# Kernel tuning notes

Hardware: AMD Instinct MI355X
Metric: run time of the kernel (lower is better)

The kernel has to match this reference:

```python
import jax, jax.numpy as jnp
import numpy as np

IH, IW = 48, 48           # img_size
C = 256                   # inp == oup
NH, HD = 8, 32            # num_heads, head_dims; inner_dim = 256
HID = 4 * C               # MLP hidden
N = IH * IW               # window size (seq len) = 2304
SCALE = (C // NH) ** -0.5 # (inp_dims // num_heads) ** -0.5
EPS = 1e-5


def _relative_position_index():
    coords = np.stack(np.meshgrid(np.arange(IH), np.arange(IW), indexing='ij'))
    cf = coords.reshape(2, -1)
    rel = (cf[:, :, None] - cf[:, None, :]).transpose(1, 2, 0)
    rel[:, :, 0] += IH - 1
    rel[:, :, 1] += IW - 1
    rel[:, :, 0] *= 2 * IW - 1
    return jnp.asarray(rel.sum(-1).astype(np.int32))  # [N, N]


def setup_inputs() -> dict:
    key = jax.random.key(0)
    ks = jax.random.split(key, 12)
    s = 0.02
    return {
        'x': jax.random.normal(ks[0], (1, IH, IW, C), jnp.float32),
        'gamma1': jnp.ones((C,), jnp.float32),
        'beta1': jnp.zeros((C,), jnp.float32),
        'w_qkv': jax.random.normal(ks[1], (C, 3 * NH * HD), jnp.float32) * s,
        'w_proj': jax.random.normal(ks[2], (NH * HD, C), jnp.float32) * s,
        'b_proj': jnp.zeros((C,), jnp.float32),
        'bias_table': jax.random.normal(ks[3], ((2 * IH - 1) * (2 * IW - 1), NH), jnp.float32) * s,
        'gamma2': jnp.ones((C,), jnp.float32),
        'beta2': jnp.zeros((C,), jnp.float32),
        'w_fc1': jax.random.normal(ks[4], (C, HID), jnp.float32) * s,
        'b_fc1': jnp.zeros((HID,), jnp.float32),
        'w_fc2': jax.random.normal(ks[5], (HID, C), jnp.float32) * s,
        'b_fc2': jnp.zeros((C,), jnp.float32),
        'rel_idx': _relative_position_index(),
    }


def _layernorm(x, g, b):
    mu = jnp.mean(x, axis=-1, keepdims=True)
    var = jnp.mean(jnp.square(x - mu), axis=-1, keepdims=True)
    return (x - mu) * jax.lax.rsqrt(var + EPS) * g + b


def reference(x, gamma1, beta1, w_qkv, w_proj, b_proj, bias_table,
              gamma2, beta2, w_fc1, b_fc1, w_fc2, b_fc2, rel_idx):
    shortcut = x                                   # [1, IH, IW, C]
    t = x.reshape(1, N, C)
    t = _layernorm(t, gamma1, beta1)

    # qkv: [1, N, 3*NH*HD] -> q, k, v each [1, NH, N, HD]
    qkv = (t @ w_qkv).reshape(1, N, 3, NH, HD).transpose(2, 0, 3, 1, 4)
    q, k, v = qkv[0], qkv[1], qkv[2]
    q = q * SCALE

    attn = jnp.einsum('bhnd,bhmd->bhnm', q, k)     # [1, NH, N, N]
    # relative position bias: gather table rows by index -> [NH, N, N]
    bias = bias_table[rel_idx.reshape(-1)].reshape(N, N, NH).transpose(2, 0, 1)
    attn = jax.nn.softmax(attn + bias[None], axis=-1)

    o = jnp.einsum('bhnm,bhmd->bhnd', attn, v)     # [1, NH, N, HD]
    o = o.transpose(0, 2, 1, 3).reshape(1, N, NH * HD)
    o = o @ w_proj + b_proj                        # [1, N, C]

    x = shortcut + o.reshape(1, IH, IW, C)
    shortcut = x

    t = _layernorm(x.reshape(1, N, C), gamma2, beta2)
    t = jax.nn.gelu(t @ w_fc1 + b_fc1, approximate=False) @ w_fc2 + b_fc2
    return shortcut + t.reshape(1, IH, IW, C)
```

## Files before the change

kernel.cpp:

```cpp
#include <hip/hip_runtime.h>
#include <hip/hip_bf16.h>
#include <math.h>

#define IH 48
#define IW 48
#define NN 2304
#define CC 256
#define NH 8
#define HD 32
#define HID 1024
#define NBIAS 9025
#define SCALE 0.17677669529663687f
#define LOG2E 1.4426950408889634f
#define LN_EPS 1e-5f

typedef __attribute__((ext_vector_type(8))) short bf16x8;
typedef __attribute__((ext_vector_type(4))) short bf16x4;
typedef __attribute__((ext_vector_type(4))) float f32x4;

__device__ __forceinline__ short f2b(float f) {
    __hip_bfloat16 h = __float2bfloat16(f);
    short s; __builtin_memcpy(&s, &h, 2); return s;
}
__device__ __forceinline__ float b2f(short s) {
    __hip_bfloat16 h; __builtin_memcpy(&h, &s, 2); return __bfloat162float(h);
}
__device__ __forceinline__ float fast_exp2(float x) {
#if __has_builtin(__builtin_amdgcn_exp2f)
    return __builtin_amdgcn_exp2f(x);
#else
    return exp2f(x);
#endif
}

__global__ void prep_kernel(const float* __restrict__ x, const float* __restrict__ g,
                            const float* __restrict__ b, short* __restrict__ t1,
                            const float* __restrict__ w_qkv, const float* __restrict__ w_proj,
                            const float* __restrict__ w_fc1, const float* __restrict__ w_fc2,
                            const float* __restrict__ bt,
                            short* __restrict__ o_qkv, short* __restrict__ o_proj,
                            short* __restrict__ o_fc1, short* __restrict__ o_fc2,
                            short* __restrict__ o_bias)
{
    const int bid = blockIdx.x, tid = threadIdx.x;
    if (bid < NN) {
        __shared__ float red[8];
        float v = x[bid * CC + tid];
        float s = v, s2 = v * v;
        #pragma unroll
        for (int off = 32; off > 0; off >>= 1) {
            s  += __shfl_xor(s, off);
            s2 += __shfl_xor(s2, off);
        }
        const int wid = tid >> 6;
        if ((tid & 63) == 0) { red[wid * 2] = s; red[wid * 2 + 1] = s2; }
        __syncthreads();
        float tot  = red[0] + red[2] + red[4] + red[6];
        float tot2 = red[1] + red[3] + red[5] + red[7];
        float mu   = tot * (1.0f / CC);
        float var  = tot2 * (1.0f / CC) - mu * mu;
        float rstd = rsqrtf(var + LN_EPS);
        t1[bid * CC + tid] = f2b((v - mu) * rstd * g[tid] + b[tid]);
        return;
    }
    const int stride = (gridDim.x - NN) * 256;
    for (int i = (bid - NN) * 256 + tid; i < 858632; i += stride) {
        int j = i;
        if (j < 196608)            { int n = j >> 8,  k = j & 255;  o_qkv [j] = f2b(w_qkv [k * 768  + n]); }
        else if ((j -= 196608) < 65536)  { int n = j >> 8,  k = j & 255;  o_proj[j] = f2b(w_proj[k * 256  + n]); }
        else if ((j -= 65536)  < 262144) { int n = j >> 8,  k = j & 255;  o_fc1 [j] = f2b(w_fc1 [k * 1024 + n]); }
        else if ((j -= 262144) < 262144) { int n = j >> 10, k = j & 1023; o_fc2 [j] = f2b(w_fc2 [k * 256  + n]); }
        else { j -= 262144; int h = j / NBIAS, idx = j - h * NBIAS; o_bias[j] = f2b(bt[idx * NH + h] * LOG2E); }
    }
}

__global__ void ln_kernel(const float* __restrict__ x,
                          const float* __restrict__ g,
                          const float* __restrict__ b,
                          short* __restrict__ out)
{
    __shared__ float red[8];
    const int row = blockIdx.x, tid = threadIdx.x;
    float v = x[row * CC + tid];
    float s = v, s2 = v * v;
    #pragma unroll
    for (int off = 32; off > 0; off >>= 1) {
        s  += __shfl_xor(s, off);
        s2 += __shfl_xor(s2, off);
    }
    const int wid = tid >> 6;
    if ((tid & 63) == 0) { red[wid * 2] = s; red[wid * 2 + 1] = s2; }
    __syncthreads();
    float tot  = red[0] + red[2] + red[4] + red[6];
    float tot2 = red[1] + red[3] + red[5] + red[7];
    float mu   = tot * (1.0f / CC);
    float var  = tot2 * (1.0f / CC) - mu * mu;
    float rstd = rsqrtf(var + LN_EPS);
    out[row * CC + tid] = f2b((v - mu) * rstd * g[tid] + b[tid]);
}

#define GSTRIDE 72
template<int K>
__device__ __forceinline__ void mfma_gemm_core(const short* __restrict__ A,
                                               const short* __restrict__ BT,
                                               int m0, int n0, f32x4 acc[4],
                                               short* lds)
{
    short* As = lds;
    short* Bs = lds + 64 * GSTRIDE;
    const int tid  = threadIdx.x;
    const int w    = tid >> 6, lane = tid & 63;
    const int quad = lane >> 4, l15 = lane & 15;
    const int sr = tid >> 2;
    const int sc = (tid & 3) * 16;
    #pragma unroll
    for (int c = 0; c < 4; ++c) acc[c] = (f32x4){0.f, 0.f, 0.f, 0.f};

    const short* Ap = &A [(m0 + sr) * K + sc];
    const short* Bp = &BT[(n0 + sr) * K + sc];
    bf16x8 ra0 = *(const bf16x8*)Ap,       ra1 = *(const bf16x8*)(Ap + 8);
    bf16x8 rb0 = *(const bf16x8*)Bp,       rb1 = *(const bf16x8*)(Bp + 8);

    for (int k0 = 0; k0 < K; k0 += 64) {
        __syncthreads();
        *(bf16x8*)&As[sr * GSTRIDE + sc]     = ra0;
        *(bf16x8*)&As[sr * GSTRIDE + sc + 8] = ra1;
        *(bf16x8*)&Bs[sr * GSTRIDE + sc]     = rb0;
        *(bf16x8*)&Bs[sr * GSTRIDE + sc + 8] = rb1;
        if (k0 + 64 < K) {
            ra0 = *(const bf16x8*)(Ap + k0 + 64);
            ra1 = *(const bf16x8*)(Ap + k0 + 72);
            rb0 = *(const bf16x8*)(Bp + k0 + 64);
            rb1 = *(const bf16x8*)(Bp + k0 + 72);
        }
        __syncthreads();
        #pragma unroll
        for (int s = 0; s < 2; ++s) {
            bf16x8 a = *(const bf16x8*)&As[(w * 16 + l15) * GSTRIDE + s * 32 + quad * 8];
            #pragma unroll
            for (int c = 0; c < 4; ++c) {
                bf16x8 b = *(const bf16x8*)&Bs[(c * 16 + l15) * GSTRIDE + s * 32 + quad * 8];
                acc[c] = __builtin_amdgcn_mfma_f32_16x16x32_bf16(a, b, acc[c], 0, 0, 0);
            }
        }
    }
}

__global__ void qkv_kernel(const short* __restrict__ t1, const short* __restrict__ wT,
                           short* __restrict__ qb, short* __restrict__ kb,
                           short* __restrict__ vT)
{
    __shared__ short lds[2 * 64 * GSTRIDE];
    f32x4 acc[4];
    const int m0 = blockIdx.y * 64, n0 = blockIdx.x * 64;
    mfma_gemm_core<256>(t1, wT, m0, n0, acc, lds);
    const int lane = threadIdx.x & 63, w = threadIdx.x >> 6;
    const int quad = lane >> 4, l15 = lane & 15;
    #pragma unroll
    for (int c = 0; c < 4; ++c) {
        int col = n0 + c * 16 + l15;
        int three = col >> 8, rem = col & 255;
        int h = rem >> 5, d = rem & 31;
        #pragma unroll
        for (int r = 0; r < 4; ++r) {
            int row = m0 + w * 16 + quad * 4 + r;
            float v = acc[c][r];
            if (three == 0)      qb[(h * NN + row) * HD + d] = f2b(v * (SCALE * LOG2E));
            else if (three == 1) kb[(h * NN + row) * HD + d] = f2b(v);
            else                 vT[(h * HD + d) * NN + row] = f2b(v);
        }
    }
}

__global__ __launch_bounds__(256) void attn_kernel(
        const short* __restrict__ qb, const short* __restrict__ kb,
        const short* __restrict__ vT, const short* __restrict__ biasT,
        short* __restrict__ o)
{
    __shared__ float Ored[4][16][33];
    __shared__ float lred[4][16];
    const int w = threadIdx.x >> 6, lane = threadIdx.x & 63;
    const int quad = lane >> 4, l15 = lane & 15;
    const int h = blockIdx.x / 144, q0 = (blockIdx.x % 144) * 16;
    const int t0 = w * 576;
    const short* bt = &biasT[h * NBIAS];

    bf16x8 qf = *(const bf16x8*)&qb[(h * NN + q0 + l15) * HD + quad * 8];

    const int qi = q0 / IW, qj = (q0 % IW) + l15;
    const int qbase = (qi + 47) * 95 + (qj + 47);

    f32x4 O0 = (f32x4){0.f,0.f,0.f,0.f}, O1 = (f32x4){0.f,0.f,0.f,0.f};
    float lp = 0.f;
    const f32x4 zero = (f32x4){0.f,0.f,0.f,0.f};

    for (int c = 0; c < 18; ++c) {
        const int t = t0 + c * 32;
        bf16x8 k0f = *(const bf16x8*)&kb[(h * NN + t      + l15) * HD + quad * 8];
        bf16x8 k1f = *(const bf16x8*)&kb[(h * NN + t + 16 + l15) * HD + quad * 8];
        const short* vp0 = &vT[(h * HD + l15)      * NN + t + quad * 4];
        const short* vp1 = &vT[(h * HD + 16 + l15) * NN + t + quad * 4];
        bf16x4 va0 = *(const bf16x4*)vp0, vb0 = *(const bf16x4*)(vp0 + 16);
        bf16x4 va1 = *(const bf16x4*)vp1, vb1 = *(const bf16x4*)(vp1 + 16);

        f32x4 s0 = __builtin_amdgcn_mfma_f32_16x16x32_bf16(k0f, qf, zero, 0, 0, 0);
        f32x4 s1 = __builtin_amdgcn_mfma_f32_16x16x32_bf16(k1f, qf, zero, 0, 0, 0);

        const int kA = t + quad * 4;
        const int kiA = kA / IW, kjA = kA % IW;
        const int kB = kA + 16;
        const int kiB = kB / IW, kjB = kB % IW;
        const short* pA = bt + (qbase - (kiA * 95 + kjA));
        const short* pB = bt + (qbase - (kiB * 95 + kjB));

        float p[8];
        #pragma unroll
        for (int r = 0; r < 4; ++r) {
            p[r]     = fast_exp2(s0[r] + b2f(pA[-r]));
            p[4 + r] = fast_exp2(s1[r] + b2f(pB[-r]));
        }
        #pragma unroll
        for (int r = 0; r < 8; ++r) lp += p[r];
        bf16x8 pa = (bf16x8){ f2b(p[0]), f2b(p[1]), f2b(p[2]), f2b(p[3]),
                              f2b(p[4]), f2b(p[5]), f2b(p[6]), f2b(p[7]) };
        bf16x8 v0 = (bf16x8){ va0[0], va0[1], va0[2], va0[3],
                              vb0[0], vb0[1], vb0[2], vb0[3] };
        bf16x8 v1 = (bf16x8){ va1[0], va1[1], va1[2], va1[3],
                              vb1[0], vb1[1], vb1[2], vb1[3] };
        O0 = __builtin_amdgcn_mfma_f32_16x16x32_bf16(pa, v0, O0, 0, 0, 0);
        O1 = __builtin_amdgcn_mfma_f32_16x16x32_bf16(pa, v1, O1, 0, 0, 0);
    }

    lp += __shfl_xor(lp, 16);
    lp += __shfl_xor(lp, 32);
    if (quad == 0) lred[w][l15] = lp;
    #pragma unroll
    for (int r = 0; r < 4; ++r) {
        Ored[w][quad * 4 + r][l15]      = O0[r];
        Ored[w][quad * 4 + r][16 + l15] = O1[r];
    }
    __syncthreads();
    {
        const int col = threadIdx.x & 31;
        for (int rr = threadIdx.x >> 5; rr < 16; rr += 8) {
            float s = 0.f, l = 0.f;
            #pragma unroll
            for (int pw = 0; pw < 4; ++pw) { s += Ored[pw][rr][col]; l += lred[pw][rr]; }
            o[(q0 + rr) * CC + h * HD + col] = f2b(s / l);
        }
    }
}

__global__ void proj_kernel(const short* __restrict__ o, const short* __restrict__ wT,
                            const float* __restrict__ bias, const float* __restrict__ x_in,
                            float* __restrict__ x2)
{
    __shared__ short lds[2 * 64 * GSTRIDE];
    f32x4 acc[4];
    const int m0 = blockIdx.y * 64, n0 = blockIdx.x * 64;
    mfma_gemm_core<256>(o, wT, m0, n0, acc, lds);
    const int lane = threadIdx.x & 63, w = threadIdx.x >> 6;
    const int quad = lane >> 4, l15 = lane & 15;
    #pragma unroll
    for (int c = 0; c < 4; ++c) {
        int col = n0 + c * 16 + l15;
        #pragma unroll
        for (int r = 0; r < 4; ++r) {
            int row = m0 + w * 16 + quad * 4 + r;
            x2[row * CC + col] = acc[c][r] + bias[col] + x_in[row * CC + col];
        }
    }
}

__global__ void fc1_kernel(const short* __restrict__ t2, const short* __restrict__ wT,
                           const float* __restrict__ bias, short* __restrict__ h1)
{
    __shared__ short lds[2 * 64 * GSTRIDE];
    f32x4 acc[4];
    const int m0 = blockIdx.y * 64, n0 = blockIdx.x * 64;
    mfma_gemm_core<256>(t2, wT, m0, n0, acc, lds);
    const int lane = threadIdx.x & 63, w = threadIdx.x >> 6;
    const int quad = lane >> 4, l15 = lane & 15;
    #pragma unroll
    for (int c = 0; c < 4; ++c) {
        int col = n0 + c * 16 + l15;
        #pragma unroll
        for (int r = 0; r < 4; ++r) {
            int row = m0 + w * 16 + quad * 4 + r;
            float v = acc[c][r] + bias[col];
            float ge = 0.5f * v * (1.0f + erff(v * 0.7071067811865476f));
            h1[row * HID + col] = f2b(ge);
        }
    }
}

__global__ void fc2_kernel(const short* __restrict__ h1, const short* __restrict__ wT,
                           const float* __restrict__ bias, const float* __restrict__ x2,
                           float* __restrict__ out)
{
    __shared__ short lds[2 * 64 * GSTRIDE];
    f32x4 acc[4];
    const int m0 = blockIdx.y * 64, n0 = blockIdx.x * 64;
    mfma_gemm_core<1024>(h1, wT, m0, n0, acc, lds);
    const int lane = threadIdx.x & 63, w = threadIdx.x >> 6;
    const int quad = lane >> 4, l15 = lane & 15;
    #pragma unroll
    for (int c = 0; c < 4; ++c) {
        int col = n0 + c * 16 + l15;
        #pragma unroll
        for (int r = 0; r < 4; ++r) {
            int row = m0 + w * 16 + quad * 4 + r;
            out[row * CC + col] = acc[c][r] + bias[col] + x2[row * CC + col];
        }
    }
}

extern "C" void kernel_launch(void* const* d_in, const int* in_sizes, int n_in,
                              void* d_out, int out_size, void* d_ws, size_t ws_size,
                              hipStream_t stream)
{
    const float* x          = (const float*)d_in[0];
    const float* gamma1     = (const float*)d_in[1];
    const float* beta1      = (const float*)d_in[2];
    const float* w_qkv      = (const float*)d_in[3];
    const float* w_proj     = (const float*)d_in[4];
    const float* b_proj     = (const float*)d_in[5];
    const float* bias_table = (const float*)d_in[6];
    const float* gamma2     = (const float*)d_in[7];
    const float* beta2      = (const float*)d_in[8];
    const float* w_fc1      = (const float*)d_in[9];
    const float* b_fc1      = (const float*)d_in[10];
    const float* w_fc2      = (const float*)d_in[11];
    const float* b_fc2      = (const float*)d_in[12];

    short* S = (short*)d_ws;
    const int NC = NN * CC;
    short* t1     = S;
    short* qb     = t1  + NC;
    short* kb     = qb  + NC;
    short* vT     = kb  + NC;
    short* obuf   = vT  + NC;
    short* t2     = obuf+ NC;
    short* h1     = t2  + NC;
    short* wTqkv  = h1  + NN * HID;
    short* wTproj = wTqkv  + 768 * 256;
    short* wTfc1  = wTproj + 256 * 256;
    short* wTfc2  = wTfc1  + 1024 * 256;
    short* biasT  = wTfc2  + 256 * 1024;
    float* x2     = (float*)(biasT + NH * NBIAS + 8);

    prep_kernel<<<NN + 512, 256, 0, stream>>>(x, gamma1, beta1, t1,
                                              w_qkv, w_proj, w_fc1, w_fc2, bias_table,
                                              wTqkv, wTproj, wTfc1, wTfc2, biasT);
    qkv_kernel<<<dim3(12, 36), 256, 0, stream>>>(t1, wTqkv, qb, kb, vT);
    attn_kernel<<<1152, 256, 0, stream>>>(qb, kb, vT, biasT, obuf);
    proj_kernel<<<dim3(4, 36), 256, 0, stream>>>(obuf, wTproj, b_proj, x, x2);
    ln_kernel<<<NN, 256, 0, stream>>>(x2, gamma2, beta2, t2);
    fc1_kernel<<<dim3(16, 36), 256, 0, stream>>>(t2, wTfc1, b_fc1, h1);
    fc2_kernel<<<dim3(4, 36), 256, 0, stream>>>(h1, wTfc2, b_fc2, x2,
                                                (float*)d_out);
}
```

Measured before the change: 187.9 us.

## Split attention key range across three blocks and reduce partials in separate kernel

The attention kernel now splits the key sequence three ways (split-K / flash-decoding style), launching three times as many blocks, each covering a third of the keys. Partial unnormalized outputs and row sums go to fp32 workspace, and a new normalization kernel sums the partials and divides. The relative-position bias table is also stored as fp32 instead of bf16, which removes the bf16-to-float conversion in the inner loop. In exchange there is an extra kernel launch, extra global traffic for the fp32 partials, and a larger bias table to read.

```diff
diff --git a/kernel.cpp b/kernel.cpp
--- a/kernel.cpp
+++ b/kernel.cpp
@@ -13,6 +13,7 @@
 #define SCALE 0.17677669529663687f
 #define LOG2E 1.4426950408889634f
 #define LN_EPS 1e-5f
+#define NSPLIT 3
 
 typedef __attribute__((ext_vector_type(8))) short bf16x8;
 typedef __attribute__((ext_vector_type(4))) short bf16x4;
@@ -40,7 +41,7 @@
                             const float* __restrict__ bt,
                             short* __restrict__ o_qkv, short* __restrict__ o_proj,
                             short* __restrict__ o_fc1, short* __restrict__ o_fc2,
-                            short* __restrict__ o_bias)
+                            float* __restrict__ o_bias)
 {
     const int bid = blockIdx.x, tid = threadIdx.x;
     if (bid < NN) {
@@ -70,7 +71,7 @@
         else if ((j -= 196608) < 65536)  { int n = j >> 8,  k = j & 255;  o_proj[j] = f2b(w_proj[k * 256  + n]); }
         else if ((j -= 65536)  < 262144) { int n = j >> 8,  k = j & 255;  o_fc1 [j] = f2b(w_fc1 [k * 1024 + n]); }
         else if ((j -= 262144) < 262144) { int n = j >> 10, k = j & 1023; o_fc2 [j] = f2b(w_fc2 [k * 256  + n]); }
-        else { j -= 262144; int h = j / NBIAS, idx = j - h * NBIAS; o_bias[j] = f2b(bt[idx * NH + h] * LOG2E); }
+        else { j -= 262144; int h = j / NBIAS, idx = j - h * NBIAS; o_bias[j] = bt[idx * NH + h] * LOG2E; }
     }
 }
 
@@ -174,16 +175,18 @@
 
 __global__ __launch_bounds__(256) void attn_kernel(
         const short* __restrict__ qb, const short* __restrict__ kb,
-        const short* __restrict__ vT, const short* __restrict__ biasT,
-        short* __restrict__ o)
+        const short* __restrict__ vT, const float* __restrict__ biasF,
+        float* __restrict__ Opart, float* __restrict__ lpart)
 {
     __shared__ float Ored[4][16][33];
     __shared__ float lred[4][16];
     const int w = threadIdx.x >> 6, lane = threadIdx.x & 63;
     const int quad = lane >> 4, l15 = lane & 15;
-    const int h = blockIdx.x / 144, q0 = (blockIdx.x % 144) * 16;
-    const int t0 = w * 576;
-    const short* bt = &biasT[h * NBIAS];
+    const int sp = blockIdx.x / 1152;
+    const int bb = blockIdx.x - sp * 1152;
+    const int h = bb / 144, q0 = (bb % 144) * 16;
+    const int t0 = sp * (NN / NSPLIT) + w * (NN / NSPLIT / 4);
+    const float* bt = &biasF[h * NBIAS];
 
     bf16x8 qf = *(const bf16x8*)&qb[(h * NN + q0 + l15) * HD + quad * 8];
 
@@ -194,7 +197,7 @@
     float lp = 0.f;
     const f32x4 zero = (f32x4){0.f,0.f,0.f,0.f};
 
-    for (int c = 0; c < 18; ++c) {
+    for (int c = 0; c < 6; ++c) {
         const int t = t0 + c * 32;
         bf16x8 k0f = *(const bf16x8*)&kb[(h * NN + t      + l15) * HD + quad * 8];
         bf16x8 k1f = *(const bf16x8*)&kb[(h * NN + t + 16 + l15) * HD + quad * 8];
@@ -207,17 +210,15 @@
         f32x4 s1 = __builtin_amdgcn_mfma_f32_16x16x32_bf16(k1f, qf, zero, 0, 0, 0);
 
         const int kA = t + quad * 4;
-        const int kiA = kA / IW, kjA = kA % IW;
         const int kB = kA + 16;
-        const int kiB = kB / IW, kjB = kB % IW;
-        const short* pA = bt + (qbase - (kiA * 95 + kjA));
-        const short* pB = bt + (qbase - (kiB * 95 + kjB));
+        const float* pA = bt + (qbase - ((kA / IW) * 95 + kA % IW));
+        const float* pB = bt + (qbase - ((kB / IW) * 95 + kB % IW));
 
         float p[8];
         #pragma unroll
         for (int r = 0; r < 4; ++r) {
-            p[r]     = fast_exp2(s0[r] + b2f(pA[-r]));
-            p[4 + r] = fast_exp2(s1[r] + b2f(pB[-r]));
+            p[r]     = fast_exp2(s0[r] + pA[-r]);
+            p[4 + r] = fast_exp2(s1[r] + pB[-r]);
         }
         #pragma unroll
         for (int r = 0; r < 8; ++r) lp += p[r];
@@ -246,9 +247,22 @@
             float s = 0.f, l = 0.f;
             #pragma unroll
             for (int pw = 0; pw < 4; ++pw) { s += Ored[pw][rr][col]; l += lred[pw][rr]; }
-            o[(q0 + rr) * CC + h * HD + col] = f2b(s / l);
-        }
-    }
+            Opart[sp * (NN * CC) + (q0 + rr) * CC + h * HD + col] = s;
+            if (col == 0) lpart[(sp * NH + h) * NN + q0 + rr] = l;
+        }
+    }
+}
+
+__global__ void attn_norm_kernel(const float* __restrict__ Opart,
+                                 const float* __restrict__ lpart,
+                                 short* __restrict__ obuf)
+{
+    const int n = blockIdx.x, c = threadIdx.x, h = c >> 5;
+    float v = Opart[n * CC + c] + Opart[NN * CC + n * CC + c]
+            + Opart[2 * NN * CC + n * CC + c];
+    float l = lpart[h * NN + n] + lpart[(NH + h) * NN + n]
+            + lpart[(2 * NH + h) * NN + n];
+    obuf[n * CC + c] = f2b(v / l);
 }
 
 __global__ void proj_kernel(const short* __restrict__ o, const short* __restrict__ wT,
@@ -346,14 +360,17 @@
     short* wTproj = wTqkv  + 768 * 256;
     short* wTfc1  = wTproj + 256 * 256;
     short* wTfc2  = wTfc1  + 1024 * 256;
-    short* biasT  = wTfc2  + 256 * 1024;
-    float* x2     = (float*)(biasT + NH * NBIAS + 8);
+    float* biasF  = (float*)(wTfc2 + 256 * 1024);
+    float* x2     = biasF + NH * NBIAS;
+    float* Opart  = x2 + NC;
+    float* lpart  = Opart + NSPLIT * NC;
 
     prep_kernel<<<NN + 512, 256, 0, stream>>>(x, gamma1, beta1, t1,
                                               w_qkv, w_proj, w_fc1, w_fc2, bias_table,
-                                              wTqkv, wTproj, wTfc1, wTfc2, biasT);
+                                              wTqkv, wTproj, wTfc1, wTfc2, biasF);
     qkv_kernel<<<dim3(12, 36), 256, 0, stream>>>(t1, wTqkv, qb, kb, vT);
-    attn_kernel<<<1152, 256, 0, stream>>>(qb, kb, vT, biasT, obuf);
+    attn_kernel<<<NSPLIT * 1152, 256, 0, stream>>>(qb, kb, vT, biasF, Opart, lpart);
+    attn_norm_kernel<<<NN, 256, 0, stream>>>(Opart, lpart, obuf);
     proj_kernel<<<dim3(4, 36), 256, 0, stream>>>(obuf, wTproj, b_proj, x, x2);
     ln_kernel<<<NN, 256, 0, stream>>>(x2, gamma2, beta2, t2);
     fc1_kernel<<<dim3(16, 36), 256, 0, stream>>>(t2, wTfc1, b_fc1, h1);
```

Result: no change. 186.1 us (-1.0%).
